# Kernel optimization log

Hardware: AMD Instinct MI355X
Metric: run time of the kernel (lower is better)

The kernel has to match this reference:

```python
import jax, jax.numpy as jnp
import numpy as np

DEPTH = 2
DIM = 1024     # shot-embedding width
SDIM = 256     # SSM state width
B = 256        # batch (episodes x classes)
S = 64         # shots per class (scan length)
EPS = 1e-5


def setup_inputs() -> dict:
    key = jax.random.key(0)
    ks = jax.random.split(key, 10)
    sc = 0.02
    return {
        "shot_embeddings": jax.random.normal(ks[0], (B, S, DIM), jnp.float32),
        # per-layer selective-scan cell params (stacked over depth)
        "Wd": jax.random.normal(ks[1], (DEPTH, DIM, SDIM), jnp.float32) * sc,   # delta proj
        "bd": jnp.zeros((DEPTH, SDIM), jnp.float32),
        "Wi": jax.random.normal(ks[2], (DEPTH, DIM, SDIM), jnp.float32) * sc,   # input (B) proj
        "bi": jnp.zeros((DEPTH, SDIM), jnp.float32),
        "A_log": jax.random.normal(ks[3], (DEPTH, SDIM), jnp.float32),          # state decay param
        "Wo": jax.random.normal(ks[4], (DEPTH, SDIM, DIM), jnp.float32) * sc,   # readout (C) proj
        "bo": jnp.zeros((DEPTH, DIM), jnp.float32),
        # state_to_class Linear(state_dim, dim) per layer
        "Ws": jax.random.normal(ks[5], (DEPTH, SDIM, DIM), jnp.float32) * sc,
        "bs": jnp.zeros((DEPTH, DIM), jnp.float32),
        # LayerNorm
        "gamma": jnp.ones((DIM,), jnp.float32),
        "beta": jnp.zeros((DIM,), jnp.float32),
    }


def _run_selective_scan(x, Wd, bd, Wi, bi, A_log, Wo, bo):
    """Mamba-style selective scan over the shot axis.
    x: [B,S,D] -> (y: [B,S,D], final_state: [B,N])"""
    delta = jax.nn.softplus(jnp.einsum('bsd,dn->bsn', x, Wd) + bd)   # [B,S,N]
    u = jnp.einsum('bsd,dn->bsn', x, Wi) + bi                        # [B,S,N]
    decay = jnp.exp(-delta * jax.nn.softplus(A_log))                 # [B,S,N]
    drive = delta * u                                                # [B,S,N]

    def step(h, t):
        d, g = t
        h = d * h + g
        return h, h

    h0 = jnp.zeros((x.shape[0], Wd.shape[1]), x.dtype)
    final, hs = jax.lax.scan(step, h0, (decay.swapaxes(0, 1), drive.swapaxes(0, 1)))
    hs = hs.swapaxes(0, 1)                                           # [B,S,N]
    y = jnp.einsum('bsn,nd->bsd', hs, Wo) + bo                       # [B,S,D]
    return y, final


def reference(shot_embeddings, Wd, bd, Wi, bi, A_log, Wo, bo, Ws, bs, gamma, beta):
    hidden = shot_embeddings
    class_state = None
    for l in range(Wd.shape[0]):  # fixed small depth
        hidden, state = _run_selective_scan(hidden, Wd[l], bd[l], Wi[l], bi[l],
                                            A_log[l], Wo[l], bo[l])
        class_state = jnp.einsum('bn,nd->bd', state, Ws[l]) + bs[l]   # [B,D]
        hidden = hidden + class_state[:, None, :]
    pooled = class_state + hidden.mean(axis=1)                        # [B,D]
    mu = pooled.mean(axis=-1, keepdims=True)
    var = pooled.var(axis=-1, keepdims=True)
    class_repr = (pooled - mu) / jnp.sqrt(var + EPS) * gamma + beta
    return class_repr, hidden
```

## Files before the change

kernel.cpp:

```cpp
#include <hip/hip_runtime.h>
#include <hip/hip_bf16.h>

#define DEPTH 2
#define DIM   1024
#define SDIM  256
#define BATCH 256
#define SHOTS 64
#define M_TOT (BATCH*SHOTS)

typedef __attribute__((ext_vector_type(8))) short bf16x8;
typedef __attribute__((ext_vector_type(4))) float f32x4;
typedef unsigned short u16;

__device__ __forceinline__ u16 f2bf(float f) {
    union { float f; unsigned u; } v; v.f = f;
    unsigned r = v.u + 0x7fffu + ((v.u >> 16) & 1u);
    return (u16)(r >> 16);
}

__device__ __forceinline__ unsigned pk_bf2(float a, float b) {
    union { __hip_bfloat162 h2; unsigned u; } c;
    c.h2 = __float22bfloat162_rn(make_float2(a, b));
    return c.u;
}

__device__ __forceinline__ float bf2f(u16 h) {
    union { unsigned u; float f; } c; c.u = (unsigned)h << 16; return c.f;
}

__device__ __forceinline__ float softplus_f(float x) {
    if (x > 15.f) return x;
    return __logf(1.f + __expf(x));
}

__device__ __forceinline__ void gld16(const u16* g, u16* l) {
    __builtin_amdgcn_global_load_lds(
        (const __attribute__((address_space(1))) unsigned int*)g,
        (__attribute__((address_space(3))) unsigned int*)l, 16, 0, 0);
}

__device__ __forceinline__ void transpose_body(
    float T[64][65], const float* __restrict__ A1, const float* __restrict__ A2,
    u16* __restrict__ out, int K, int SPLIT, int k0, int n0, int destbase,
    int layer, int N, int tid)
{
    const bool first = (n0 < SPLIT);
    const int scols = first ? SPLIT : (N - SPLIT);
    const float* S = (first ? A1 : A2) + (size_t)layer * K * scols
                     + (first ? n0 : (n0 - SPLIT));
    out += (size_t)layer * K * N;

    #pragma unroll
    for (int i = 0; i < 4; ++i) {
        const int c = tid + i * 256;
        const int kr = c >> 4, cc = c & 15;
        const float4 v = *(const float4*)(S + (size_t)(k0 + kr) * scols + cc * 4);
        T[kr][cc * 4 + 0] = v.x; T[kr][cc * 4 + 1] = v.y;
        T[kr][cc * 4 + 2] = v.z; T[kr][cc * 4 + 3] = v.w;
    }
    __syncthreads();
    #pragma unroll
    for (int i = 0; i < 4; ++i) {
        const int c = tid + i * 256;
        const int nr = c >> 4, cc = c & 15;
        ushort4 h;
        h.x = f2bf(T[cc * 4 + 0][nr]); h.y = f2bf(T[cc * 4 + 1][nr]);
        h.z = f2bf(T[cc * 4 + 2][nr]); h.w = f2bf(T[cc * 4 + 3][nr]);
        *(ushort4*)&out[(size_t)(destbase + nr) * K + k0 + cc * 4] = h;
    }
}

__global__ __launch_bounds__(256)
void prep(const float* __restrict__ Wd, const float* __restrict__ Wi,
          const float* __restrict__ Wo, const float* __restrict__ Ws,
          const float* __restrict__ X0,
          u16* __restrict__ WcombT, u16* __restrict__ WoT,
          u16* __restrict__ Wsb, u16* __restrict__ Xbf)
{
    __shared__ float T[64][65];
    const int bid = blockIdx.x;
    const int tid = threadIdx.x;

    if (bid < 256) {
        const int kx = bid & 15, ny = (bid >> 4) & 7, lz = bid >> 7;
        const int n0 = ny * 64;
        const int destbase = (n0 < 256) ? (n0 >> 6) * 128
                                        : ((n0 - 256) >> 6) * 128 + 64;
        transpose_body(T, Wd, Wi, WcombT, 1024, 256, kx * 64, n0, destbase,
                       lz, 512, tid);
    } else if (bid < 384) {
        const int sub = bid - 256;
        const int kx = sub & 3, ny = (sub >> 2) & 15, lz = sub >> 6;
        transpose_body(T, Wo, Wo, WoT, 256, 1024, kx * 64, ny * 64, ny * 64,
                       lz, 1024, tid);
    } else if (bid < 640) {
        const size_t i = ((size_t)(bid - 384) * 256 + tid) * 8;
        const float4 a = *(const float4*)(Ws + i);
        const float4 b = *(const float4*)(Ws + i + 4);
        int4 o;
        o.x = (int)pk_bf2(a.x, a.y); o.y = (int)pk_bf2(a.z, a.w);
        o.z = (int)pk_bf2(b.x, b.y); o.w = (int)pk_bf2(b.z, b.w);
        *(int4*)(Wsb + i) = o;
    } else {
        const size_t total = (size_t)M_TOT * DIM;
        const size_t stride = (size_t)2048 * 256 * 8;
        for (size_t i = ((size_t)(bid - 640) * 256 + tid) * 8; i < total; i += stride) {
            const float4 a = *(const float4*)(X0 + i);
            const float4 b = *(const float4*)(X0 + i + 4);
            int4 o;
            o.x = (int)pk_bf2(a.x, a.y); o.y = (int)pk_bf2(a.z, a.w);
            o.z = (int)pk_bf2(b.x, b.y); o.w = (int)pk_bf2(b.z, b.w);
            *(int4*)(Xbf + i) = o;
        }
    }
}

#define BM 128
#define BN 128
#define BK 64


__global__ __launch_bounds__(256)
void gemm_pq_scan(const u16* __restrict__ A, const u16* __restrict__ BT,
                  const float* __restrict__ bd, const float* __restrict__ bi,
                  const float* __restrict__ A_log,
                  u16* __restrict__ hsb, float* __restrict__ stateb, int CB)
{
    __shared__ __align__(16) char pool[35072];
    u16* As = (u16*)pool;
    u16* Bs = (u16*)(pool + 16384);
    float (*Ct)[129]  = (float(*)[129])pool;
    float2 (*grp)[64] = (float2(*)[64])(pool + 33024);

    const int tid = threadIdx.x;
    const int id  = blockIdx.x;
    const int xcd = id & 7, slot = id >> 3;
    const int rb = xcd + 8 * (slot / CB);
    const int cb = slot % CB;
    const int row0 = rb * BM, col0 = cb * BN;
    const int K = 1024;

    const int l  = tid & 63;
    const int w  = tid >> 6;
    const int wm = (w >> 1) * 64, wn = (w & 1) * 64;
    const int lr = l & 15, lq = l >> 4;

    const int srow = w * 8 + (l >> 3);
    const int scol = (l & 7) * 8;
    const u16* Ag = A  + (size_t)(row0 + srow) * K + scol;
    const u16* Bg = BT + (size_t)(col0 + srow) * K + scol;
    u16* Asd = &As[(w * 64 + l) * 8];
    u16* Bsd = &Bs[(w * 64 + l) * 8];

    f32x4 acc[4][4];
    #pragma unroll
    for (int i = 0; i < 4; ++i)
        #pragma unroll
        for (int j = 0; j < 4; ++j)
            acc[i][j] = (f32x4){0.f, 0.f, 0.f, 0.f};

    for (int k0 = 0; k0 < K; k0 += BK) {
        #pragma unroll
        for (int i = 0; i < 4; ++i) {
            gld16(Ag + (size_t)(i * 32) * K + k0, Asd + i * 2048);
            gld16(Bg + (size_t)(i * 32) * K + k0, Bsd + i * 2048);
        }
        __syncthreads();

        #pragma unroll
        for (int ks = 0; ks < 2; ++ks) {
            bf16x8 af[4], bfr[4];
            #pragma unroll
            for (int i = 0; i < 4; ++i)
                af[i] = *(const bf16x8*)&As[(wm + i * 16 + lr) * BK + ks * 32 + lq * 8];
            #pragma unroll
            for (int j = 0; j < 4; ++j)
                bfr[j] = *(const bf16x8*)&Bs[(wn + j * 16 + lr) * BK + ks * 32 + lq * 8];
            #pragma unroll
            for (int i = 0; i < 4; ++i)
                #pragma unroll
                for (int j = 0; j < 4; ++j)
                    acc[i][j] = __builtin_amdgcn_mfma_f32_16x16x32_bf16(
                        af[i], bfr[j], acc[i][j], 0, 0, 0);
        }
        __syncthreads();
    }

    const int n0  = cb * 64;
    const int seg = tid >> 6;
    const int nl  = tid & 63;
    const int n   = n0 + nl;
    const float bdv = bd[n], biv = bi[n];
    const float spA = softplus_f(A_log[n]);

    for (int bl = 0; bl < 2; ++bl) {
        if (bl) __syncthreads();
        if ((w >> 1) == bl) {
            #pragma unroll
            for (int i = 0; i < 4; ++i)
                #pragma unroll
                for (int j = 0; j < 4; ++j)
                    #pragma unroll
                    for (int r = 0; r < 4; ++r)
                        Ct[i * 16 + lq * 4 + r][wn + j * 16 + lr] = acc[i][j][r];
        }
        __syncthreads();

        float a = 1.f, hl = 0.f;
        #pragma unroll
        for (int s2 = 0; s2 < 16; ++s2) {
            const int s = seg * 16 + s2;
            const float delta = softplus_f(Ct[s][nl] + bdv);
            const float d  = __expf(-delta * spA);
            const float gv = delta * (Ct[s][64 + nl] + biv);
            Ct[s][nl] = d; Ct[s][64 + nl] = gv;
            a *= d; hl = d * hl + gv;
        }
        grp[seg][nl] = make_float2(a, hl);
        __syncthreads();

        float h = 0.f;
        for (int j = 0; j < seg; ++j) {
            const float2 sv = grp[j][nl];
            h = sv.x * h + sv.y;
        }

        const int b = 2 * rb + bl;
        u16* hout = hsb + ((size_t)b * SHOTS + seg * 16) * SDIM + n;
        #pragma unroll
        for (int s2 = 0; s2 < 16; ++s2) {
            const int s = seg * 16 + s2;
            h = Ct[s][nl] * h + Ct[s][64 + nl];
            hout[(size_t)s2 * SDIM] = f2bf(h);
        }
        if (seg == 3) stateb[(size_t)b * SDIM + n] = h;
    }
}

template<bool BF16OUT, bool POOL>
__global__ __launch_bounds__(256)
void gemm_hidden(const u16* __restrict__ A, const u16* __restrict__ BT,
                 void* __restrict__ Cv, const float* __restrict__ bo,
                 const float* __restrict__ bs, const u16* __restrict__ Wsb,
                 const float* __restrict__ stateb, float* __restrict__ pooled,
                 float* __restrict__ csbuf, int CB)
{
    __shared__ __align__(16) u16 As[BM * BK];
    __shared__ __align__(16) u16 Bs[BN * BK];
    __shared__ float stL[512];
    __shared__ float csL[2][128];

    const int tid = threadIdx.x;
    const int id  = blockIdx.x;
    const int xcd = id & 7, slot = id >> 3;
    const int rb = xcd + 8 * (slot / CB);
    const int cb = slot % CB;
    const int row0 = rb * BM, col0 = cb * BN;
    const int K = 256, ldc = DIM;
    const int b0 = row0 >> 6;

    stL[tid]       = stateb[(size_t)b0 * SDIM + tid];
    stL[tid + 256] = stateb[(size_t)b0 * SDIM + tid + 256];

    const int l  = tid & 63;
    const int w  = tid >> 6;
    const int wm = (w >> 1) * 64, wn = (w & 1) * 64;
    const int lr = l & 15, lq = l >> 4;

    const int srow = w * 8 + (l >> 3);
    const int scol = (l & 7) * 8;
    const u16* Ag = A  + (size_t)(row0 + srow) * K + scol;
    const u16* Bg = BT + (size_t)(col0 + srow) * K + scol;
    u16* Asd = &As[(w * 64 + l) * 8];
    u16* Bsd = &Bs[(w * 64 + l) * 8];

    f32x4 acc[4][4];
    #pragma unroll
    for (int i = 0; i < 4; ++i)
        #pragma unroll
        for (int j = 0; j < 4; ++j)
            acc[i][j] = (f32x4){0.f, 0.f, 0.f, 0.f};

    for (int k0 = 0; k0 < K; k0 += BK) {
        #pragma unroll
        for (int i = 0; i < 4; ++i) {
            gld16(Ag + (size_t)(i * 32) * K + k0, Asd + i * 2048);
            gld16(Bg + (size_t)(i * 32) * K + k0, Bsd + i * 2048);
        }
        __syncthreads();

        #pragma unroll
        for (int ks = 0; ks < 2; ++ks) {
            bf16x8 af[4], bfr[4];
            #pragma unroll
            for (int i = 0; i < 4; ++i)
                af[i] = *(const bf16x8*)&As[(wm + i * 16 + lr) * BK + ks * 32 + lq * 8];
            #pragma unroll
            for (int j = 0; j < 4; ++j)
                bfr[j] = *(const bf16x8*)&Bs[(wn + j * 16 + lr) * BK + ks * 32 + lq * 8];
            #pragma unroll
            for (int i = 0; i < 4; ++i)
                #pragma unroll
                for (int j = 0; j < 4; ++j)
                    acc[i][j] = __builtin_amdgcn_mfma_f32_16x16x32_bf16(
                        af[i], bfr[j], acc[i][j], 0, 0, 0);
        }
        __syncthreads();
    }

    {
        const int kq = tid >> 6, blc = (tid >> 5) & 1, cg = tid & 31;
        const int kb = kq * 64;
        f32x4 part = {0.f, 0.f, 0.f, 0.f};
        #pragma unroll 8
        for (int k = 0; k < 64; ++k) {
            const float sk = stL[blc * 256 + kb + k];
            const ushort4 wv = *(const ushort4*)
                &Wsb[(size_t)(kb + k) * DIM + col0 + cg * 4];
            part[0] += sk * bf2f(wv.x); part[1] += sk * bf2f(wv.y);
            part[2] += sk * bf2f(wv.z); part[3] += sk * bf2f(wv.w);
        }
        f32x4* psumL = (f32x4*)As;
        psumL[tid] = part;
        __syncthreads();
        if (tid < 64) {
            const int bl2 = tid >> 5, cg2 = tid & 31;
            f32x4 s = psumL[bl2 * 32 + cg2];
            #pragma unroll
            for (int kq2 = 1; kq2 < 4; ++kq2)
                s += psumL[kq2 * 64 + bl2 * 32 + cg2];
            const float4 bv = *(const float4*)(bs + col0 + cg2 * 4);
            float4 o;
            o.x = s[0] + bv.x; o.y = s[1] + bv.y;
            o.z = s[2] + bv.z; o.w = s[3] + bv.w;
            *(float4*)&csL[bl2][cg2 * 4] = o;
            *(float4*)(csbuf + (size_t)(b0 + bl2) * DIM + col0 + cg2 * 4) = o;
        }
        __syncthreads();
    }

    float psum[4] = {0.f, 0.f, 0.f, 0.f};
    #pragma unroll
    for (int i = 0; i < 4; ++i) {
        const int grow = row0 + wm + i * 16 + lq * 4;
        const int bl = (grow >> 6) & 1;
        #pragma unroll
        for (int j = 0; j < 4; ++j) {
            const int gcol = col0 + wn + j * 16 + lr;
            const float addv = bo[gcol] + csL[bl][gcol - col0];
            #pragma unroll
            for (int r = 0; r < 4; ++r) {
                const float val = acc[i][j][r] + addv;
                if (BF16OUT) ((u16*)Cv)[(size_t)(grow + r) * ldc + gcol] = f2bf(val);
                else         ((float*)Cv)[(size_t)(grow + r) * ldc + gcol] = val;
                if (POOL) psum[j] += val;
            }
        }
    }
    if (POOL) {
        const int batch_w = (row0 + wm) >> 6;
        #pragma unroll
        for (int j = 0; j < 4; ++j) {
            float v = psum[j];
            v += __shfl_xor(v, 16, 64);
            v += __shfl_xor(v, 32, 64);
            if (lq == 0)
                pooled[(size_t)batch_w * DIM + col0 + wn + j * 16 + lr] = v;
        }
    }
}

__global__ __launch_bounds__(1024)
void final_kernel(const float* __restrict__ pooled, const float* __restrict__ cs,
                  const float* __restrict__ gamma, const float* __restrict__ beta,
                  float* __restrict__ out)
{
    const int b = blockIdx.x;
    const int d = threadIdx.x;

    const float p = cs[(size_t)b * DIM + d]
                  + pooled[(size_t)b * DIM + d] * (1.f / SHOTS);

    __shared__ float rsum[1024], rsq[1024];
    rsum[d] = p; rsq[d] = p * p;
    __syncthreads();
    for (int off = 512; off > 0; off >>= 1) {
        if (d < off) { rsum[d] += rsum[d + off]; rsq[d] += rsq[d + off]; }
        __syncthreads();
    }
    const float mu  = rsum[0] * (1.f / DIM);
    const float var = rsq[0] * (1.f / DIM) - mu * mu;
    const float inv = rsqrtf(var + 1e-5f);

    out[(size_t)b * DIM + d] = (p - mu) * inv * gamma[d] + beta[d];
}


extern "C" void kernel_launch(void* const* d_in, const int* in_sizes, int n_in,
                              void* d_out, int out_size, void* d_ws, size_t ws_size,
                              hipStream_t stream)
{
    const float* X0    = (const float*)d_in[0];
    const float* Wd    = (const float*)d_in[1];
    const float* bd    = (const float*)d_in[2];
    const float* Wi    = (const float*)d_in[3];
    const float* bi    = (const float*)d_in[4];
    const float* A_log = (const float*)d_in[5];
    const float* Wo    = (const float*)d_in[6];
    const float* bo    = (const float*)d_in[7];
    const float* Ws    = (const float*)d_in[8];
    const float* bs    = (const float*)d_in[9];
    const float* gamma = (const float*)d_in[10];
    const float* beta  = (const float*)d_in[11];

    float* out_cr     = (float*)d_out;
    float* out_hidden = out_cr + (size_t)BATCH * DIM;

    u16* Xbf = (u16*)out_hidden;

    char* w = (char*)d_ws;
    float*  csbuf  = (float*)w;  w += (size_t)BATCH * DIM * 4;
    float*  pooled = (float*)w;  w += (size_t)BATCH * DIM * 4;
    float*  stateb = (float*)w;  w += (size_t)BATCH * SDIM * 4;
    u16*    hsb    = (u16*)w;    w += (size_t)M_TOT * SDIM * 2;
    u16*    WcombT = (u16*)w;    w += (size_t)DEPTH * 512 * 1024 * 2;
    u16*    WoT    = (u16*)w;    w += (size_t)DEPTH * 1024 * 256 * 2;
    u16*    Wsb    = (u16*)w;    w += (size_t)DEPTH * SDIM * DIM * 2;

    prep<<<2688, 256, 0, stream>>>(Wd, Wi, Wo, Ws, X0, WcombT, WoT, Wsb, Xbf);

    for (int l = 0; l < DEPTH; ++l) {
        gemm_pq_scan<<<512, 256, 0, stream>>>(
            Xbf, WcombT + (size_t)l * 512 * 1024,
            bd + l * SDIM, bi + l * SDIM, A_log + l * SDIM,
            hsb, stateb, 4);
        if (l < DEPTH - 1) {
            gemm_hidden<true, false><<<1024, 256, 0, stream>>>(
                hsb, WoT + (size_t)l * 1024 * 256, Xbf, bo + l * DIM,
                bs + l * DIM, Wsb + (size_t)l * SDIM * DIM, stateb,
                nullptr, csbuf, 8);
        } else {
            gemm_hidden<false, true><<<1024, 256, 0, stream>>>(
                hsb, WoT + (size_t)l * 1024 * 256, out_hidden, bo + l * DIM,
                bs + l * DIM, Wsb + (size_t)l * SDIM * DIM, stateb,
                pooled, csbuf, 8);
        }
    }
    final_kernel<<<BATCH, 1024, 0, stream>>>(pooled, csbuf, gamma, beta, out_cr);
}
```

Before: 256.5 us.

## Fold layer-0 readout into layer-1 input projection to skip hidden GEMM

Layer 1's delta/input projections are applied to hidden0 = hs0·Wo0 + bo0 + cs0. The change precomputes the fused weight Wo0·[Wd1|Wi1] (256x512) in prep. Layer 1 then runs a K=256 GEMM directly on the layer-0 states, adding a per-batch-row correction (bo0 + state·Ws0 + bs0) projected through Wd1/Wi1. This removes the full layer-0 hidden GEMM (M=16384, N=1024, K=256) and the K=1024 projection, replacing them with a K=256 GEMM plus small per-row matvecs. It adds an fp32 fused-weight computation in prep, a per-block 1024-long dot product in the scan kernel prologue, and bf16 rounding of the fused weights, which shifts numerics.

Result: slower. 327.8 us (+27.8%).

```diff
diff --git a/kernel.cpp b/kernel.cpp
--- a/kernel.cpp
+++ b/kernel.cpp
@@ -75,9 +75,10 @@
           const float* __restrict__ Wo, const float* __restrict__ Ws,
           const float* __restrict__ X0,
           u16* __restrict__ WcombT, u16* __restrict__ WoT,
-          u16* __restrict__ Wsb, u16* __restrict__ Xbf)
+          u16* __restrict__ Wsb, u16* __restrict__ WfT, u16* __restrict__ Xbf)
 {
     __shared__ float T[64][65];
+    __shared__ float WoL[4][1024];
     const int bid = blockIdx.x;
     const int tid = threadIdx.x;
 
@@ -101,10 +102,43 @@
         o.x = (int)pk_bf2(a.x, a.y); o.y = (int)pk_bf2(a.z, a.w);
         o.z = (int)pk_bf2(b.x, b.y); o.w = (int)pk_bf2(b.z, b.w);
         *(int4*)(Wsb + i) = o;
+    } else if (bid < 704) {
+        const int k4 = (bid - 640) * 4;
+        #pragma unroll
+        for (int i = 0; i < 4; ++i) {
+            const int idx = tid + i * 256;
+            const int r = idx >> 8, c4 = (idx & 255) * 4;
+            *(float4*)&WoL[r][c4] = *(const float4*)(Wo + (size_t)(k4 + r) * 1024 + c4);
+        }
+        __syncthreads();
+        const int np0 = 2 * tid;
+        const float* Wd1 = Wd + (size_t)1024 * 256;
+        const float* Wi1 = Wi + (size_t)1024 * 256;
+        const float* Wsrc = (np0 < 256) ? (Wd1 + np0) : (Wi1 + (np0 - 256));
+        float acc[4][2] = {};
+        #pragma unroll 4
+        for (int d = 0; d < 1024; ++d) {
+            const float2 wv = *(const float2*)(Wsrc + (size_t)d * 256);
+            #pragma unroll
+            for (int r = 0; r < 4; ++r) {
+                const float a = WoL[r][d];
+                acc[r][0] += a * wv.x; acc[r][1] += a * wv.y;
+            }
+        }
+        #pragma unroll
+        for (int j = 0; j < 2; ++j) {
+            const int np = np0 + j;
+            int rr;
+            if (np < 256) rr = (np >> 6) * 128 + (np & 63);
+            else { const int m = np - 256; rr = (m >> 6) * 128 + 64 + (m & 63); }
+            #pragma unroll
+            for (int r = 0; r < 4; ++r)
+                WfT[(size_t)rr * 256 + k4 + r] = f2bf(acc[r][j]);
+        }
     } else {
         const size_t total = (size_t)M_TOT * DIM;
         const size_t stride = (size_t)2048 * 256 * 8;
-        for (size_t i = ((size_t)(bid - 640) * 256 + tid) * 8; i < total; i += stride) {
+        for (size_t i = ((size_t)(bid - 704) * 256 + tid) * 8; i < total; i += stride) {
             const float4 a = *(const float4*)(X0 + i);
             const float4 b = *(const float4*)(X0 + i + 4);
             int4 o;
@@ -115,15 +149,40 @@
     }
 }
 
+__global__ __launch_bounds__(256)
+void csrow(const float* __restrict__ stateb, const u16* __restrict__ Wsb0,
+           const float* __restrict__ bs0, const float* __restrict__ bo0,
+           float* __restrict__ rbuf)
+{
+    __shared__ float stL[SDIM];
+    const int b = blockIdx.x, tid = threadIdx.x;
+    stL[tid] = stateb[(size_t)b * SDIM + tid];
+    __syncthreads();
+    const int d0 = tid * 4;
+    const float4 b1 = *(const float4*)(bs0 + d0);
+    const float4 b2 = *(const float4*)(bo0 + d0);
+    f32x4 acc = {b1.x + b2.x, b1.y + b2.y, b1.z + b2.z, b1.w + b2.w};
+    #pragma unroll 8
+    for (int k = 0; k < SDIM; ++k) {
+        const float sk = stL[k];
+        const ushort4 wv = *(const ushort4*)&Wsb0[(size_t)k * DIM + d0];
+        acc[0] += sk * bf2f(wv.x); acc[1] += sk * bf2f(wv.y);
+        acc[2] += sk * bf2f(wv.z); acc[3] += sk * bf2f(wv.w);
+    }
+    *(f32x4*)(rbuf + (size_t)b * DIM + d0) = acc;
+}
+
 #define BM 128
 #define BN 128
 #define BK 64
 
-
+template<int KK, bool HAS_T>
 __global__ __launch_bounds__(256)
 void gemm_pq_scan(const u16* __restrict__ A, const u16* __restrict__ BT,
                   const float* __restrict__ bd, const float* __restrict__ bi,
                   const float* __restrict__ A_log,
+                  const float* __restrict__ rbuf, const float* __restrict__ Wd1,
+                  const float* __restrict__ Wi1,
                   u16* __restrict__ hsb, float* __restrict__ stateb, int CB)
 {
     __shared__ __align__(16) char pool[35072];
@@ -131,6 +190,7 @@
     u16* Bs = (u16*)(pool + 16384);
     float (*Ct)[129]  = (float(*)[129])pool;
     float2 (*grp)[64] = (float2(*)[64])(pool + 33024);
+    __shared__ float Tlds[2][128];
 
     const int tid = threadIdx.x;
     const int id  = blockIdx.x;
@@ -138,12 +198,24 @@
     const int rb = xcd + 8 * (slot / CB);
     const int cb = slot % CB;
     const int row0 = rb * BM, col0 = cb * BN;
-    const int K = 1024;
+    const int K = KK;
 
     const int l  = tid & 63;
     const int w  = tid >> 6;
     const int wm = (w >> 1) * 64, wn = (w & 1) * 64;
     const int lr = l & 15, lq = l >> 4;
+
+    if (HAS_T) {
+        const int bl = tid >> 7, c = tid & 127;
+        const float* rrow = rbuf + (size_t)(2 * rb + bl) * DIM;
+        const float* Wcol = (c < 64) ? (Wd1 + (cb * 64 + c))
+                                     : (Wi1 + (cb * 64 + (c - 64)));
+        float acc = 0.f;
+        #pragma unroll 8
+        for (int d = 0; d < DIM; ++d)
+            acc += rrow[d] * Wcol[(size_t)d * SDIM];
+        Tlds[bl][c] = acc;
+    }
 
     const int srow = w * 8 + (l >> 3);
     const int scol = (l & 7) * 8;
@@ -206,13 +278,16 @@
         }
         __syncthreads();
 
+        const float tp = HAS_T ? Tlds[bl][nl] : 0.f;
+        const float tq = HAS_T ? Tlds[bl][64 + nl] : 0.f;
+
         float a = 1.f, hl = 0.f;
         #pragma unroll
         for (int s2 = 0; s2 < 16; ++s2) {
             const int s = seg * 16 + s2;
-            const float delta = softplus_f(Ct[s][nl] + bdv);
+            const float delta = softplus_f(Ct[s][nl] + tp + bdv);
             const float d  = __expf(-delta * spA);
-            const float gv = delta * (Ct[s][64 + nl] + biv);
+            const float gv = delta * (Ct[s][64 + nl] + tq + biv);
             Ct[s][nl] = d; Ct[s][64 + nl] = gv;
             a *= d; hl = d * hl + gv;
         }
@@ -422,29 +497,34 @@
     float*  csbuf  = (float*)w;  w += (size_t)BATCH * DIM * 4;
     float*  pooled = (float*)w;  w += (size_t)BATCH * DIM * 4;
     float*  stateb = (float*)w;  w += (size_t)BATCH * SDIM * 4;
+    float*  rbuf   = (float*)w;  w += (size_t)BATCH * DIM * 4;
     u16*    hsb    = (u16*)w;    w += (size_t)M_TOT * SDIM * 2;
+    u16*    hsb2   = (u16*)w;    w += (size_t)M_TOT * SDIM * 2;
     u16*    WcombT = (u16*)w;    w += (size_t)DEPTH * 512 * 1024 * 2;
     u16*    WoT    = (u16*)w;    w += (size_t)DEPTH * 1024 * 256 * 2;
     u16*    Wsb    = (u16*)w;    w += (size_t)DEPTH * SDIM * DIM * 2;
-
-    prep<<<2688, 256, 0, stream>>>(Wd, Wi, Wo, Ws, X0, WcombT, WoT, Wsb, Xbf);
-
-    for (int l = 0; l < DEPTH; ++l) {
-        gemm_pq_scan<<<512, 256, 0, stream>>>(
-            Xbf, WcombT + (size_t)l * 512 * 1024,
-            bd + l * SDIM, bi + l * SDIM, A_log + l * SDIM,
-            hsb, stateb, 4);
-        if (l < DEPTH - 1) {
-            gemm_hidden<true, false><<<1024, 256, 0, stream>>>(
-                hsb, WoT + (size_t)l * 1024 * 256, Xbf, bo + l * DIM,
-                bs + l * DIM, Wsb + (size_t)l * SDIM * DIM, stateb,
-                nullptr, csbuf, 8);
-        } else {
-            gemm_hidden<false, true><<<1024, 256, 0, stream>>>(
-                hsb, WoT + (size_t)l * 1024 * 256, out_hidden, bo + l * DIM,
-                bs + l * DIM, Wsb + (size_t)l * SDIM * DIM, stateb,
-                pooled, csbuf, 8);
-        }
-    }
+    u16*    WfT    = (u16*)w;    w += (size_t)512 * 256 * 2;
+
+    const float* Wd1 = Wd + (size_t)1024 * 256;
+    const float* Wi1 = Wi + (size_t)1024 * 256;
+
+    prep<<<2752, 256, 0, stream>>>(Wd, Wi, Wo, Ws, X0,
+                                   WcombT, WoT, Wsb, WfT, Xbf);
+
+    gemm_pq_scan<1024, false><<<512, 256, 0, stream>>>(
+        Xbf, WcombT, bd, bi, A_log,
+        nullptr, nullptr, nullptr, hsb, stateb, 4);
+
+    csrow<<<BATCH, 256, 0, stream>>>(stateb, Wsb, bs, bo, rbuf);
+
+    gemm_pq_scan<256, true><<<512, 256, 0, stream>>>(
+        hsb, WfT, bd + SDIM, bi + SDIM, A_log + SDIM,
+        rbuf, Wd1, Wi1, hsb2, stateb, 4);
+
+    gemm_hidden<false, true><<<1024, 256, 0, stream>>>(
+        hsb2, WoT + (size_t)1024 * 256, out_hidden, bo + DIM,
+        bs + DIM, Wsb + (size_t)SDIM * DIM, stateb,
+        pooled, csbuf, 8);
+
     final_kernel<<<BATCH, 1024, 0, stream>>>(pooled, csbuf, gamma, beta, out_cr);
 }
```
